# Performance work log

Measured on AMD Instinct MI355X. Metric: run time of the kernel, lower is better.

The kernel has to match this reference:

```python
import jax, jax.numpy as jnp
import numpy as np

N_HEADS = 16


def setup_inputs() -> dict:
    key = jax.random.key(0)
    k1, k2, k3 = jax.random.split(key, 3)
    B, T, D = 2, 2048, 1024
    x = jax.random.normal(k1, (B, T, D), dtype=jnp.float32)
    w_qkv = jax.random.normal(k2, (3 * D, D), dtype=jnp.float32) * 0.02
    w_proj = jax.random.normal(k3, (D, D), dtype=jnp.float32) * (0.02 / np.sqrt(24.0))
    return {"x": x, "w_qkv": w_qkv, "w_proj": w_proj}


def reference(x, w_qkv, w_proj):
    B, T, D = x.shape
    H = N_HEADS
    dh = D // H
    # qkv linear (no bias): x @ w_qkv.T -> [B, T, 3D]
    qkv = jnp.einsum('btd,ed->bte', x, w_qkv)
    q, k, v = jnp.split(qkv, 3, axis=-1)
    q = q.reshape(B, T, H, dh)
    k = k.reshape(B, T, H, dh)
    v = v.reshape(B, T, H, dh)
    # attention with materialized scores [B, H, T, S]
    scores = jnp.einsum('bthd,bshd->bhts', q, k) / jnp.sqrt(jnp.asarray(dh, x.dtype))
    attn = jax.nn.softmax(scores.astype(jnp.float32), axis=-1).astype(x.dtype)
    out = jnp.einsum('bhts,bshd->bthd', attn, v).reshape(B, T, D)
    # output projection (no bias)
    return jnp.einsum('btd,ed->bte', out, w_proj)
```

## Files before the change

### kernel.cpp

```cpp
#include <hip/hip_runtime.h>


typedef __attribute__((ext_vector_type(8))) short s8v;
typedef __attribute__((ext_vector_type(8))) unsigned short us8;
typedef __attribute__((ext_vector_type(4))) unsigned short us4;
typedef __attribute__((ext_vector_type(4))) float f4v;
typedef __attribute__((ext_vector_type(16))) float f16v;
typedef __attribute__((ext_vector_type(4))) unsigned u4v;

__device__ __forceinline__ unsigned short f2b(float f) {
    unsigned u = __builtin_bit_cast(unsigned, f);
    u += 0x7FFFu + ((u >> 16) & 1u);
    return (unsigned short)(u >> 16);
}
__device__ __forceinline__ unsigned packtrunc(float a, float b, unsigned sel) {
    unsigned r;
    asm("v_perm_b32 %0, %1, %2, %3"
        : "=v"(r)
        : "v"(__builtin_bit_cast(unsigned, b)), "v"(__builtin_bit_cast(unsigned, a)), "s"(sel));
    return r;
}

#if __has_builtin(__builtin_amdgcn_exp2f)
#define EXP2F(x) __builtin_amdgcn_exp2f(x)
#else
#define EXP2F(x) exp2f(x)
#endif

#define QSCALE 0.18033688011112042f

__global__ __launch_bounds__(256) void cvt_all(const float* __restrict__ x,
                                               const float* __restrict__ wq,
                                               const float* __restrict__ wp,
                                               unsigned short* __restrict__ xb,
                                               unsigned short* __restrict__ wqb,
                                               unsigned short* __restrict__ wpb) {
    const int nx = 4096 * 1024 / 4, nq = 3072 * 1024 / 4;
    int i = blockIdx.x * 256 + threadIdx.x;
    const float* s;
    unsigned short* d;
    int j;
    if (i < nx)           { s = x;  d = xb;  j = i; }
    else if (i < nx + nq) { s = wq; d = wqb; j = i - nx; }
    else                  { s = wp; d = wpb; j = i - nx - nq; }
    float4 v = ((const float4*)s)[j];
    ushort4 o;
    o.x = f2b(v.x); o.y = f2b(v.y); o.z = f2b(v.z); o.w = f2b(v.w);
    ((ushort4*)d)[j] = o;
}

#define GLD_LDS16(g, l)                                                                        \
    __builtin_amdgcn_global_load_lds((const __attribute__((address_space(1))) unsigned*)(g),   \
                                     (__attribute__((address_space(3))) unsigned*)(l), 16, 0, 0)

__global__ __launch_bounds__(256) void gemm_qkv(const unsigned short* __restrict__ A,
                                                const unsigned short* __restrict__ B,
                                                unsigned short* __restrict__ qkvb) {
    __shared__ unsigned short As[128][64];
    __shared__ unsigned short Bs[128][64];
    const int tid = threadIdx.x;
    const int l = tid & 63, w = tid >> 6;
    const int quad = l >> 4, ln = l & 15;
    const int m0 = blockIdx.y * 128, n0 = blockIdx.x * 128;
    const int wm = (w >> 1) * 64, wn = (w & 1) * 64;

    const f4v fz = {0.f, 0.f, 0.f, 0.f};
    f4v acc[4][4];
#pragma unroll
    for (int i = 0; i < 4; ++i)
#pragma unroll
        for (int j = 0; j < 4; ++j) acc[i][j] = fz;

    const int srow = tid >> 3, sc8 = tid & 7;
    const int gcol = ((sc8 ^ (srow & 7)) << 3);
    const int koff0 = ((quad ^ (ln & 7)) << 3);
    const int koff1 = (((4 + quad) ^ (ln & 7)) << 3);

    for (int k0 = 0; k0 < 1024; k0 += 64) {
#pragma unroll
        for (int b = 0; b < 4; ++b) {
            GLD_LDS16(A + (size_t)(m0 + srow + 32 * b) * 1024 + k0 + gcol, &As[srow + 32 * b][sc8 * 8]);
            GLD_LDS16(B + (size_t)(n0 + srow + 32 * b) * 1024 + k0 + gcol, &Bs[srow + 32 * b][sc8 * 8]);
        }
        __syncthreads();
#pragma unroll
        for (int ks = 0; ks < 2; ++ks) {
            const int ko = ks ? koff1 : koff0;
            s8v af[4], bf[4];
#pragma unroll
            for (int mt = 0; mt < 4; ++mt) af[mt] = *(const s8v*)&As[wm + mt * 16 + ln][ko];
#pragma unroll
            for (int nt = 0; nt < 4; ++nt) bf[nt] = *(const s8v*)&Bs[wn + nt * 16 + ln][ko];
#pragma unroll
            for (int mt = 0; mt < 4; ++mt)
#pragma unroll
                for (int nt = 0; nt < 4; ++nt)
                    acc[mt][nt] = __builtin_amdgcn_mfma_f32_16x16x32_bf16(af[mt], bf[nt], acc[mt][nt], 0, 0, 0);
        }
        __syncthreads();
    }

#pragma unroll
    for (int mt = 0; mt < 4; ++mt)
#pragma unroll
        for (int nt = 0; nt < 4; ++nt) {
            const int col = n0 + wn + nt * 16 + ln;
            const int row = m0 + wm + mt * 16 + quad * 4;
            const float sc = (col < 1024) ? QSCALE : 1.0f;
#pragma unroll
            for (int r = 0; r < 4; ++r)
                qkvb[(size_t)(row + r) * 3072 + col] = f2b(acc[mt][nt][r] * sc);
        }
}

__global__ __launch_bounds__(256) void gemm_proj(const unsigned short* __restrict__ A,
                                                 const unsigned short* __restrict__ B,
                                                 float* __restrict__ C) {
    __shared__ unsigned short As[128][64];
    __shared__ unsigned short Bs[64][64];
    const int tid = threadIdx.x;
    const int l = tid & 63, w = tid >> 6;
    const int quad = l >> 4, ln = l & 15;
    const int m0 = blockIdx.y * 128, n0 = blockIdx.x * 64;
    const int wm = w * 32;

    const f4v fz = {0.f, 0.f, 0.f, 0.f};
    f4v acc[2][4];
#pragma unroll
    for (int i = 0; i < 2; ++i)
#pragma unroll
        for (int j = 0; j < 4; ++j) acc[i][j] = fz;

    const int srow = tid >> 3, sc8 = tid & 7;
    const int gcol = ((sc8 ^ (srow & 7)) << 3);
    const int koff0 = ((quad ^ (ln & 7)) << 3);
    const int koff1 = (((4 + quad) ^ (ln & 7)) << 3);

    for (int k0 = 0; k0 < 1024; k0 += 64) {
#pragma unroll
        for (int b = 0; b < 4; ++b)
            GLD_LDS16(A + (size_t)(m0 + srow + 32 * b) * 1024 + k0 + gcol, &As[srow + 32 * b][sc8 * 8]);
#pragma unroll
        for (int b = 0; b < 2; ++b)
            GLD_LDS16(B + (size_t)(n0 + srow + 32 * b) * 1024 + k0 + gcol, &Bs[srow + 32 * b][sc8 * 8]);
        __syncthreads();
#pragma unroll
        for (int ks = 0; ks < 2; ++ks) {
            const int ko = ks ? koff1 : koff0;
            s8v af[2], bf[4];
#pragma unroll
            for (int mt = 0; mt < 2; ++mt) af[mt] = *(const s8v*)&As[wm + mt * 16 + ln][ko];
#pragma unroll
            for (int nt = 0; nt < 4; ++nt) bf[nt] = *(const s8v*)&Bs[nt * 16 + ln][ko];
#pragma unroll
            for (int mt = 0; mt < 2; ++mt)
#pragma unroll
                for (int nt = 0; nt < 4; ++nt)
                    acc[mt][nt] = __builtin_amdgcn_mfma_f32_16x16x32_bf16(af[mt], bf[nt], acc[mt][nt], 0, 0, 0);
        }
        __syncthreads();
    }

#pragma unroll
    for (int mt = 0; mt < 2; ++mt)
#pragma unroll
        for (int nt = 0; nt < 4; ++nt) {
            const int row = m0 + wm + mt * 16 + quad * 4;
            const int col = n0 + nt * 16 + ln;
#pragma unroll
            for (int r = 0; r < 4; ++r) C[(size_t)(row + r) * 1024 + col] = acc[mt][nt][r];
        }
}


__global__ __launch_bounds__(256) void attn_split(const unsigned short* __restrict__ qkvb,
                                                  float* __restrict__ opart,
                                                  float* __restrict__ lpart) {
    __shared__ unsigned short Ks[2][64][76];
    __shared__ unsigned short Vt[2][64][76];

    const int tid = threadIdx.x;
    const int l = tid & 63, w = tid >> 6;
    const int m31 = l & 31, h2 = l >> 5;
    const int qw = w * 32;
    const int t0 = blockIdx.x * 128;
    const int hh = blockIdx.y;
    const int bb = blockIdx.z >> 1, sp = blockIdx.z & 1;
    const size_t rowbase = (size_t)bb * 2048;
    const int sbase = sp * 1024;
    const unsigned sel = 0x07060302u;

#pragma unroll
    for (int it = 0; it < 4; ++it) {
        const int idx = tid + it * 256;
        const int qr = idx >> 3, qc = (idx & 7) * 8;
        unsigned short* dst = (qr < 64) ? &Ks[0][qr][qc] : &Ks[1][qr - 64][qc];
        *(us8*)dst = *(const us8*)(qkvb + (rowbase + t0 + qr) * 3072 + hh * 64 + qc);
    }
    __syncthreads();
    s8v qf[4];
    {
        const int qrow = qw + m31;
#pragma unroll
        for (int k4 = 0; k4 < 4; ++k4)
            qf[k4] = (qrow < 64) ? *(const s8v*)&Ks[0][qrow][k4 * 16 + h2 * 8]
                                 : *(const s8v*)&Ks[1][qrow - 64][k4 * 16 + h2 * 8];
    }
    __syncthreads();

    const int r0 = tid >> 3, c0 = (tid & 7) * 8;
    const int va = tid >> 4, vc = tid & 15;

    f16v zz;
#pragma unroll
    for (int i = 0; i < 16; ++i) zz[i] = 0.f;
    f16v oacc[2];
    oacc[0] = zz; oacc[1] = zz;
    float lsum = 0.f;

    us8 kreg0 = *(const us8*)(qkvb + (rowbase + sbase + r0) * 3072 + 1024 + hh * 64 + c0);
    us8 kreg1 = *(const us8*)(qkvb + (rowbase + sbase + r0 + 32) * 3072 + 1024 + hh * 64 + c0);
    us4 vreg[4];
#pragma unroll
    for (int j = 0; j < 4; ++j)
        vreg[j] = *(const us4*)(qkvb + (rowbase + sbase + 4 * va + j) * 3072 + 2048 + hh * 64 + 4 * vc);
    *(us8*)&Ks[0][r0][c0] = kreg0;
    *(us8*)&Ks[0][r0 + 32][c0] = kreg1;
#pragma unroll
    for (int dd = 0; dd < 4; ++dd) {
        unsigned lo = (unsigned)vreg[0][dd] | ((unsigned)vreg[1][dd] << 16);
        unsigned hi = (unsigned)vreg[2][dd] | ((unsigned)vreg[3][dd] << 16);
        uint2 pk2; pk2.x = lo; pk2.y = hi;
        *(uint2*)&Vt[0][4 * vc + dd][4 * va] = pk2;
    }

    for (int i = 0; i < 16; ++i) {
        const int cur = i & 1;
        __syncthreads();

        if (i + 1 < 16) {
            const int sn = sbase + (i + 1) * 64;
            kreg0 = *(const us8*)(qkvb + (rowbase + sn + r0) * 3072 + 1024 + hh * 64 + c0);
            kreg1 = *(const us8*)(qkvb + (rowbase + sn + r0 + 32) * 3072 + 1024 + hh * 64 + c0);
#pragma unroll
            for (int j = 0; j < 4; ++j)
                vreg[j] = *(const us4*)(qkvb + (rowbase + sn + 4 * va + j) * 3072 + 2048 + hh * 64 + 4 * vc);
        }

        f16v sacc[2];
        sacc[0] = zz; sacc[1] = zz;
#pragma unroll
        for (int k4 = 0; k4 < 4; ++k4) {
#pragma unroll
            for (int st = 0; st < 2; ++st) {
                s8v kf = *(const s8v*)&Ks[cur][st * 32 + m31][k4 * 16 + h2 * 8];
                sacc[st] = __builtin_amdgcn_mfma_f32_32x32x16_bf16(kf, qf[k4], sacc[st], 0, 0, 0);
            }
        }

        unsigned wv[2][4][2];
#pragma unroll
        for (int st = 0; st < 2; ++st)
#pragma unroll
            for (int g = 0; g < 4; ++g) {
                float p0 = EXP2F(sacc[st][g * 4 + 0]);
                float p1 = EXP2F(sacc[st][g * 4 + 1]);
                float p2 = EXP2F(sacc[st][g * 4 + 2]);
                float p3 = EXP2F(sacc[st][g * 4 + 3]);
                lsum += (p0 + p1) + (p2 + p3);
                wv[st][g][0] = packtrunc(p0, p1, sel);
                wv[st][g][1] = packtrunc(p2, p3, sel);
            }

        s8v pf[4];
#pragma unroll
        for (int st = 0; st < 2; ++st)
#pragma unroll
            for (int e = 0; e < 2; ++e) {
                auto ra = __builtin_amdgcn_permlane32_swap(wv[st][2 * e][0], wv[st][2 * e + 1][0], false, false);
                auto rb = __builtin_amdgcn_permlane32_swap(wv[st][2 * e][1], wv[st][2 * e + 1][1], false, false);
                u4v t;
                t[0] = ra[0]; t[1] = rb[0];
                t[2] = ra[1]; t[3] = rb[1];
                pf[2 * st + e] = __builtin_bit_cast(s8v, t);
            }

#pragma unroll
        for (int k2 = 0; k2 < 4; ++k2) {
#pragma unroll
            for (int nt = 0; nt < 2; ++nt) {
                s8v vfr = *(const s8v*)&Vt[cur][nt * 32 + m31][k2 * 16 + h2 * 8];
                oacc[nt] = __builtin_amdgcn_mfma_f32_32x32x16_bf16(pf[k2], vfr, oacc[nt], 0, 0, 0);
            }
        }

        if (i + 1 < 16) {
            *(us8*)&Ks[1 - cur][r0][c0] = kreg0;
            *(us8*)&Ks[1 - cur][r0 + 32][c0] = kreg1;
#pragma unroll
            for (int dd = 0; dd < 4; ++dd) {
                unsigned lo = (unsigned)vreg[0][dd] | ((unsigned)vreg[1][dd] << 16);
                unsigned hi = (unsigned)vreg[2][dd] | ((unsigned)vreg[3][dd] << 16);
                uint2 pk2; pk2.x = lo; pk2.y = hi;
                *(uint2*)&Vt[1 - cur][4 * vc + dd][4 * va] = pk2;
            }
        }
    }

    lsum += __shfl_xor(lsum, 32, 64);
    if (h2 == 0)
        lpart[((size_t)sp * 4096 + rowbase + t0 + qw + m31) * 16 + hh] = lsum;

    float* op = opart + (size_t)sp * 4096 * 1024;
#pragma unroll
    for (int nt = 0; nt < 2; ++nt)
#pragma unroll
        for (int g = 0; g < 4; ++g)
#pragma unroll
            for (int r = 0; r < 4; ++r) {
                const int qrow = 8 * g + 4 * h2 + r;
                op[(rowbase + t0 + qw + qrow) * 1024 + hh * 64 + nt * 32 + m31] = oacc[nt][g * 4 + r];
            }
}

__global__ __launch_bounds__(256) void attn_combine(const float* __restrict__ opart,
                                                    const float* __restrict__ lpart,
                                                    unsigned short* __restrict__ attnb) {
    const int idx = blockIdx.x * 256 + threadIdx.x;
    const int r = idx >> 8, c4 = (idx & 255) << 2, h = c4 >> 6;
    const size_t fi = (size_t)r * 256 + (c4 >> 2);
    float4 o0 = ((const float4*)opart)[fi];
    float4 o1 = ((const float4*)(opart + (size_t)4096 * 1024))[fi];
    float ls = lpart[(size_t)r * 16 + h] + lpart[((size_t)4096 + r) * 16 + h];
    float s = 1.001955f / ls;
    ushort4 o;
    o.x = f2b((o0.x + o1.x) * s);
    o.y = f2b((o0.y + o1.y) * s);
    o.z = f2b((o0.z + o1.z) * s);
    o.w = f2b((o0.w + o1.w) * s);
    ((ushort4*)attnb)[fi] = o;
}

__global__ __launch_bounds__(256) void attn_mfma(const unsigned short* __restrict__ qkvb,
                                                 unsigned short* __restrict__ attnb) {
    __shared__ unsigned short Ks[2][64][76];
    __shared__ unsigned short Vt[2][64][76];
    __shared__ float lred[128];

    const int tid = threadIdx.x;
    const int l = tid & 63, w = tid >> 6;
    const int m31 = l & 31, h2 = l >> 5;
    const int qw = w * 32;
    const int t0 = blockIdx.x * 128;
    const int hh = blockIdx.y, bb = blockIdx.z;
    const size_t rowbase = (size_t)bb * 2048;
    const unsigned sel = 0x07060302u;

#pragma unroll
    for (int it = 0; it < 4; ++it) {
        const int idx = tid + it * 256;
        const int qr = idx >> 3, qc = (idx & 7) * 8;
        unsigned short* dst = (qr < 64) ? &Ks[0][qr][qc] : &Ks[1][qr - 64][qc];
        *(us8*)dst = *(const us8*)(qkvb + (rowbase + t0 + qr) * 3072 + hh * 64 + qc);
    }
    __syncthreads();
    s8v qf[4];
    {
        const int qrow = qw + m31;
#pragma unroll
        for (int k4 = 0; k4 < 4; ++k4)
            qf[k4] = (qrow < 64) ? *(const s8v*)&Ks[0][qrow][k4 * 16 + h2 * 8]
                                 : *(const s8v*)&Ks[1][qrow - 64][k4 * 16 + h2 * 8];
    }
    __syncthreads();

    const int r0 = tid >> 3, c0 = (tid & 7) * 8;
    const int va = tid >> 4, vc = tid & 15;

    f16v zz;
#pragma unroll
    for (int i = 0; i < 16; ++i) zz[i] = 0.f;
    f16v oacc[2];
    oacc[0] = zz; oacc[1] = zz;
    float lsum = 0.f;

    us8 kreg0 = *(const us8*)(qkvb + (rowbase + r0) * 3072 + 1024 + hh * 64 + c0);
    us8 kreg1 = *(const us8*)(qkvb + (rowbase + r0 + 32) * 3072 + 1024 + hh * 64 + c0);
    us4 vreg[4];
#pragma unroll
    for (int j = 0; j < 4; ++j)
        vreg[j] = *(const us4*)(qkvb + (rowbase + 4 * va + j) * 3072 + 2048 + hh * 64 + 4 * vc);
    *(us8*)&Ks[0][r0][c0] = kreg0;
    *(us8*)&Ks[0][r0 + 32][c0] = kreg1;
#pragma unroll
    for (int dd = 0; dd < 4; ++dd) {
        unsigned lo = (unsigned)vreg[0][dd] | ((unsigned)vreg[1][dd] << 16);
        unsigned hi = (unsigned)vreg[2][dd] | ((unsigned)vreg[3][dd] << 16);
        uint2 pk2; pk2.x = lo; pk2.y = hi;
        *(uint2*)&Vt[0][4 * vc + dd][4 * va] = pk2;
    }

    for (int i = 0; i < 32; ++i) {
        const int cur = i & 1;
        __syncthreads();

        if (i + 1 < 32) {
            const int sn = (i + 1) * 64;
            kreg0 = *(const us8*)(qkvb + (rowbase + sn + r0) * 3072 + 1024 + hh * 64 + c0);
            kreg1 = *(const us8*)(qkvb + (rowbase + sn + r0 + 32) * 3072 + 1024 + hh * 64 + c0);
#pragma unroll
            for (int j = 0; j < 4; ++j)
                vreg[j] = *(const us4*)(qkvb + (rowbase + sn + 4 * va + j) * 3072 + 2048 + hh * 64 + 4 * vc);
        }

        f16v sacc[2];
        sacc[0] = zz; sacc[1] = zz;
#pragma unroll
        for (int k4 = 0; k4 < 4; ++k4) {
#pragma unroll
            for (int st = 0; st < 2; ++st) {
                s8v kf = *(const s8v*)&Ks[cur][st * 32 + m31][k4 * 16 + h2 * 8];
                sacc[st] = __builtin_amdgcn_mfma_f32_32x32x16_bf16(kf, qf[k4], sacc[st], 0, 0, 0);
            }
        }

        unsigned wv[2][4][2];
#pragma unroll
        for (int st = 0; st < 2; ++st)
#pragma unroll
            for (int g = 0; g < 4; ++g) {
                float p0 = EXP2F(sacc[st][g * 4 + 0]);
                float p1 = EXP2F(sacc[st][g * 4 + 1]);
                float p2 = EXP2F(sacc[st][g * 4 + 2]);
                float p3 = EXP2F(sacc[st][g * 4 + 3]);
                lsum += (p0 + p1) + (p2 + p3);
                wv[st][g][0] = packtrunc(p0, p1, sel);
                wv[st][g][1] = packtrunc(p2, p3, sel);
            }

        s8v pf[4];
#pragma unroll
        for (int st = 0; st < 2; ++st)
#pragma unroll
            for (int e = 0; e < 2; ++e) {
                auto ra = __builtin_amdgcn_permlane32_swap(wv[st][2 * e][0], wv[st][2 * e + 1][0], false, false);
                auto rb = __builtin_amdgcn_permlane32_swap(wv[st][2 * e][1], wv[st][2 * e + 1][1], false, false);
                u4v t;
                t[0] = ra[0]; t[1] = rb[0];
                t[2] = ra[1]; t[3] = rb[1];
                pf[2 * st + e] = __builtin_bit_cast(s8v, t);
            }

#pragma unroll
        for (int k2 = 0; k2 < 4; ++k2) {
#pragma unroll
            for (int nt = 0; nt < 2; ++nt) {
                s8v vfr = *(const s8v*)&Vt[cur][nt * 32 + m31][k2 * 16 + h2 * 8];
                oacc[nt] = __builtin_amdgcn_mfma_f32_32x32x16_bf16(pf[k2], vfr, oacc[nt], 0, 0, 0);
            }
        }

        if (i + 1 < 32) {
            *(us8*)&Ks[1 - cur][r0][c0] = kreg0;
            *(us8*)&Ks[1 - cur][r0 + 32][c0] = kreg1;
#pragma unroll
            for (int dd = 0; dd < 4; ++dd) {
                unsigned lo = (unsigned)vreg[0][dd] | ((unsigned)vreg[1][dd] << 16);
                unsigned hi = (unsigned)vreg[2][dd] | ((unsigned)vreg[3][dd] << 16);
                uint2 pk2; pk2.x = lo; pk2.y = hi;
                *(uint2*)&Vt[1 - cur][4 * vc + dd][4 * va] = pk2;
            }
        }
    }

    lsum += __shfl_xor(lsum, 32, 64);
    lred[qw + m31] = lsum;
    float inv[16];
#pragma unroll
    for (int g = 0; g < 4; ++g)
#pragma unroll
        for (int r = 0; r < 4; ++r)
            inv[g * 4 + r] = 1.001955f / lred[qw + 8 * g + 4 * h2 + r];

#pragma unroll
    for (int nt = 0; nt < 2; ++nt)
#pragma unroll
        for (int g = 0; g < 4; ++g)
#pragma unroll
            for (int r = 0; r < 4; ++r) {
                const int qrow = 8 * g + 4 * h2 + r;
                float o = oacc[nt][g * 4 + r] * inv[g * 4 + r];
                attnb[(rowbase + t0 + qw + qrow) * 1024 + hh * 64 + nt * 32 + m31] = f2b(o);
            }
}

extern "C" void kernel_launch(void* const* d_in, const int* in_sizes, int n_in,
                              void* d_out, int out_size, void* d_ws, size_t ws_size,
                              hipStream_t stream) {
    const float* x      = (const float*)d_in[0];
    const float* w_qkv  = (const float*)d_in[1];
    const float* w_proj = (const float*)d_in[2];
    float* out = (float*)d_out;

    char* p = (char*)d_ws;
    unsigned short* xb    = (unsigned short*)p;  p += (size_t)4096 * 1024 * 2;
    unsigned short* wqb   = (unsigned short*)p;  p += (size_t)3072 * 1024 * 2;
    unsigned short* wpb   = (unsigned short*)p;  p += (size_t)1024 * 1024 * 2;
    unsigned short* qkvb  = (unsigned short*)p;  p += (size_t)4096 * 3072 * 2;
    unsigned short* attnb = (unsigned short*)p;  p += (size_t)4096 * 1024 * 2;
    float* opart = (float*)p;  p += (size_t)2 * 4096 * 1024 * 4;
    float* lpart = (float*)p;  p += (size_t)2 * 4096 * 16 * 4;
    const size_t need = (size_t)(p - (char*)d_ws);

    cvt_all<<<8192, 256, 0, stream>>>(x, w_qkv, w_proj, xb, wqb, wpb);

    gemm_qkv<<<dim3(3072 / 128, 4096 / 128), 256, 0, stream>>>(xb, wqb, qkvb);

    if (ws_size >= need) {
        attn_split<<<dim3(2048 / 128, 16, 4), 256, 0, stream>>>(qkvb, opart, lpart);
        attn_combine<<<4096, 256, 0, stream>>>(opart, lpart, attnb);
    } else {
        attn_mfma<<<dim3(2048 / 128, 16, 2), 256, 0, stream>>>(qkvb, attnb);
    }

    gemm_proj<<<dim3(1024 / 64, 4096 / 128), 256, 0, stream>>>(attnb, wpb, out);
}
```

Before: 198.8 us.

## Load K tiles directly to LDS with XOR swizzle and interleave score/PV per subtile

Replaces the register-staged K tile loads with direct global-to-LDS loads (GLD_LDS16) into an unpadded, XOR-swizzled K buffer, and reads K fragments with the matching swizzle. The score, exp and PV stages are restructured to run per 32-row subtile, which lowers live registers, and launch bounds now request 4 blocks per CU. The aim is to cut VGPR pressure and LDS store instructions and to raise occupancy. It depends on the GLD_LDS16 macro defined elsewhere and on the async LDS writes being complete before the barrier.

```diff
diff --git a/kernel.cpp b/kernel.cpp
--- a/kernel.cpp
+++ b/kernel.cpp
@@ -172,11 +172,10 @@
         }
 }
 
-
-__global__ __launch_bounds__(256) void attn_split(const unsigned short* __restrict__ qkvb,
-                                                  float* __restrict__ opart,
-                                                  float* __restrict__ lpart) {
-    __shared__ unsigned short Ks[2][64][76];
+__global__ __launch_bounds__(256, 4) void attn_split(const unsigned short* __restrict__ qkvb,
+                                                     float* __restrict__ opart,
+                                                     float* __restrict__ lpart) {
+    __shared__ unsigned short Ks[2][64][64];
     __shared__ unsigned short Vt[2][64][76];
 
     const int tid = threadIdx.x;
@@ -208,8 +207,13 @@
     }
     __syncthreads();
 
-    const int r0 = tid >> 3, c0 = (tid & 7) * 8;
+    const int r0 = tid >> 3, sc8 = tid & 7;
+    const int kgcol = ((sc8 ^ (r0 & 7)) << 3);
     const int va = tid >> 4, vc = tid & 15;
+    const int kxor = (m31 & 7);
+
+    const unsigned short* kb = qkvb + 1024 + hh * 64 + kgcol;
+    const unsigned short* vb = qkvb + 2048 + hh * 64 + 4 * vc;
 
     f16v zz;
 #pragma unroll
@@ -218,14 +222,12 @@
     oacc[0] = zz; oacc[1] = zz;
     float lsum = 0.f;
 
-    us8 kreg0 = *(const us8*)(qkvb + (rowbase + sbase + r0) * 3072 + 1024 + hh * 64 + c0);
-    us8 kreg1 = *(const us8*)(qkvb + (rowbase + sbase + r0 + 32) * 3072 + 1024 + hh * 64 + c0);
+    GLD_LDS16(kb + (size_t)(rowbase + sbase + r0) * 3072, &Ks[0][r0][sc8 * 8]);
+    GLD_LDS16(kb + (size_t)(rowbase + sbase + r0 + 32) * 3072, &Ks[0][r0 + 32][sc8 * 8]);
     us4 vreg[4];
 #pragma unroll
     for (int j = 0; j < 4; ++j)
-        vreg[j] = *(const us4*)(qkvb + (rowbase + sbase + 4 * va + j) * 3072 + 2048 + hh * 64 + 4 * vc);
-    *(us8*)&Ks[0][r0][c0] = kreg0;
-    *(us8*)&Ks[0][r0 + 32][c0] = kreg1;
+        vreg[j] = *(const us4*)(vb + (size_t)(rowbase + sbase + 4 * va + j) * 3072);
 #pragma unroll
     for (int dd = 0; dd < 4; ++dd) {
         unsigned lo = (unsigned)vreg[0][dd] | ((unsigned)vreg[1][dd] << 16);
@@ -239,64 +241,51 @@
         __syncthreads();
 
         if (i + 1 < 16) {
-            const int sn = sbase + (i + 1) * 64;
-            kreg0 = *(const us8*)(qkvb + (rowbase + sn + r0) * 3072 + 1024 + hh * 64 + c0);
-            kreg1 = *(const us8*)(qkvb + (rowbase + sn + r0 + 32) * 3072 + 1024 + hh * 64 + c0);
+            const size_t sn = rowbase + sbase + (i + 1) * 64;
+            GLD_LDS16(kb + (sn + r0) * 3072, &Ks[1 - cur][r0][sc8 * 8]);
+            GLD_LDS16(kb + (sn + r0 + 32) * 3072, &Ks[1 - cur][r0 + 32][sc8 * 8]);
 #pragma unroll
             for (int j = 0; j < 4; ++j)
-                vreg[j] = *(const us4*)(qkvb + (rowbase + sn + 4 * va + j) * 3072 + 2048 + hh * 64 + 4 * vc);
-        }
-
-        f16v sacc[2];
-        sacc[0] = zz; sacc[1] = zz;
-#pragma unroll
-        for (int k4 = 0; k4 < 4; ++k4) {
-#pragma unroll
-            for (int st = 0; st < 2; ++st) {
-                s8v kf = *(const s8v*)&Ks[cur][st * 32 + m31][k4 * 16 + h2 * 8];
-                sacc[st] = __builtin_amdgcn_mfma_f32_32x32x16_bf16(kf, qf[k4], sacc[st], 0, 0, 0);
-            }
-        }
-
-        unsigned wv[2][4][2];
-#pragma unroll
-        for (int st = 0; st < 2; ++st)
+                vreg[j] = *(const us4*)(vb + (sn + 4 * va + j) * 3072);
+        }
+
+#pragma unroll
+        for (int st = 0; st < 2; ++st) {
+            f16v sacc = zz;
+#pragma unroll
+            for (int k4 = 0; k4 < 4; ++k4) {
+                s8v kf = *(const s8v*)&Ks[cur][st * 32 + m31][((2 * k4 + h2) ^ kxor) << 3];
+                sacc = __builtin_amdgcn_mfma_f32_32x32x16_bf16(kf, qf[k4], sacc, 0, 0, 0);
+            }
+            unsigned wv[4][2];
 #pragma unroll
             for (int g = 0; g < 4; ++g) {
-                float p0 = EXP2F(sacc[st][g * 4 + 0]);
-                float p1 = EXP2F(sacc[st][g * 4 + 1]);
-                float p2 = EXP2F(sacc[st][g * 4 + 2]);
-                float p3 = EXP2F(sacc[st][g * 4 + 3]);
+                float p0 = EXP2F(sacc[g * 4 + 0]);
+                float p1 = EXP2F(sacc[g * 4 + 1]);
+                float p2 = EXP2F(sacc[g * 4 + 2]);
+                float p3 = EXP2F(sacc[g * 4 + 3]);
                 lsum += (p0 + p1) + (p2 + p3);
-                wv[st][g][0] = packtrunc(p0, p1, sel);
-                wv[st][g][1] = packtrunc(p2, p3, sel);
-            }
-
-        s8v pf[4];
-#pragma unroll
-        for (int st = 0; st < 2; ++st)
+                wv[g][0] = packtrunc(p0, p1, sel);
+                wv[g][1] = packtrunc(p2, p3, sel);
+            }
 #pragma unroll
             for (int e = 0; e < 2; ++e) {
-                auto ra = __builtin_amdgcn_permlane32_swap(wv[st][2 * e][0], wv[st][2 * e + 1][0], false, false);
-                auto rb = __builtin_amdgcn_permlane32_swap(wv[st][2 * e][1], wv[st][2 * e + 1][1], false, false);
+                auto ra = __builtin_amdgcn_permlane32_swap(wv[2 * e][0], wv[2 * e + 1][0], false, false);
+                auto rb = __builtin_amdgcn_permlane32_swap(wv[2 * e][1], wv[2 * e + 1][1], false, false);
                 u4v t;
                 t[0] = ra[0]; t[1] = rb[0];
                 t[2] = ra[1]; t[3] = rb[1];
-                pf[2 * st + e] = __builtin_bit_cast(s8v, t);
-            }
-
-#pragma unroll
-        for (int k2 = 0; k2 < 4; ++k2) {
-#pragma unroll
-            for (int nt = 0; nt < 2; ++nt) {
-                s8v vfr = *(const s8v*)&Vt[cur][nt * 32 + m31][k2 * 16 + h2 * 8];
-                oacc[nt] = __builtin_amdgcn_mfma_f32_32x32x16_bf16(pf[k2], vfr, oacc[nt], 0, 0, 0);
+                s8v pf = __builtin_bit_cast(s8v, t);
+                const int k2 = 2 * st + e;
+#pragma unroll
+                for (int nt = 0; nt < 2; ++nt) {
+                    s8v vfr = *(const s8v*)&Vt[cur][nt * 32 + m31][k2 * 16 + h2 * 8];
+                    oacc[nt] = __builtin_amdgcn_mfma_f32_32x32x16_bf16(pf, vfr, oacc[nt], 0, 0, 0);
+                }
             }
         }
 
         if (i + 1 < 16) {
-            *(us8*)&Ks[1 - cur][r0][c0] = kreg0;
-            *(us8*)&Ks[1 - cur][r0 + 32][c0] = kreg1;
 #pragma unroll
             for (int dd = 0; dd < 4; ++dd) {
                 unsigned lo = (unsigned)vreg[0][dd] | ((unsigned)vreg[1][dd] << 16);
```

Result: faster. 192.3 us (-3.3%).
